# Optimization experiments

Measured on AMD Instinct MI355X. Metric: run time of the kernel, lower is better.

## Reference

```python
import jax, jax.numpy as jnp
import numpy as np

BATCH = 131072
INPUT_DIM = 256
HIDDEN = 128
DIM = 16
TRIL = DIM * (DIM + 1) // 2  # 136


def setup_inputs() -> dict:
    key = jax.random.key(0)
    k_x, k_w1, k_w2 = jax.random.split(key, 3)
    x = jax.random.normal(k_x, (BATCH, INPUT_DIM), dtype=jnp.float32)
    # Kaiming-ish init scaling so activations are well-conditioned
    W1 = jax.random.normal(k_w1, (INPUT_DIM, HIDDEN), dtype=jnp.float32) * (1.0 / np.sqrt(INPUT_DIM))
    b1 = jnp.zeros((HIDDEN,), dtype=jnp.float32)
    W2 = jax.random.normal(k_w2, (HIDDEN, TRIL), dtype=jnp.float32) * (1.0 / np.sqrt(HIDDEN))
    b2 = jnp.zeros((TRIL,), dtype=jnp.float32)
    return {"x": x, "W1": W1, "b1": b1, "W2": W2, "b2": b2}


def reference(x, W1, b1, W2, b2):
    # MLP: Linear -> ReLU -> Linear, producing tril entries of Cholesky factor
    h = jax.nn.relu(x @ W1 + b1)              # [B, 128]
    v = h @ W2 + b2                           # [B, 136]
    ti, tj = jnp.tril_indices(DIM)            # row-major tril order, matches torch.tril_indices
    L = jnp.zeros((x.shape[0], DIM, DIM), dtype=v.dtype).at[:, ti, tj].set(v)  # [B, D, D]
    rho = jnp.einsum('bik,bjk->bij', L, L)    # L @ L^T (real, so conj is no-op)
    trace = jnp.einsum('bii->b', rho)         # diagonal sum
    return rho / trace[:, None, None]
```

## Files before the change

kernel.cpp:

```cpp
#include <hip/hip_runtime.h>


typedef _Float16 h8 __attribute__((ext_vector_type(8)));
typedef float    f4 __attribute__((ext_vector_type(4)));
typedef int      i2 __attribute__((ext_vector_type(2)));

#define BATCH_N 131072
#define IN_DIM  256
#define HID     128
#define TRILN   136
#define BM      128
#define NT1     8
#define KS1     8
#define NT2     9
#define KS2     4
#define HSTR    136
#define LVSTR   160
#define PW1_N   (KS1*NT1*64*8)
#define PW2_N   (KS2*NT2*64*8)

__device__ __forceinline__ int rowoff(int i) {
    int g = i >> 2;
    return 4 * (g + 1) * (2 * g + (i & 3));
}

__global__ void pack_weights(const float* __restrict__ W1,
                             const float* __restrict__ W2,
                             _Float16* __restrict__ pw1,
                             _Float16* __restrict__ pw2) {
    int gid = blockIdx.x * blockDim.x + threadIdx.x;
    if (gid < PW1_N) {
        int j = gid & 7, l = (gid >> 3) & 63, f = gid >> 9;
        int ks = f >> 3, nt = f & 7;
        int k = ks * 32 + (l >> 4) * 8 + j;
        int n = nt * 16 + (l & 15);
        pw1[gid] = (_Float16)W1[k * HID + n];
    } else if (gid < PW1_N + PW2_N) {
        int g = gid - PW1_N;
        int j = g & 7, l = (g >> 3) & 63, f = g >> 9;
        int ks = f / NT2, nt = f - ks * NT2;
        int k = ks * 32 + (l >> 4) * 8 + j;
        int col = nt * 16 + (l & 15);
        pw2[g] = (col < TRILN) ? (_Float16)W2[k * TRILN + col] : (_Float16)0.0f;
    }
}

__device__ __forceinline__ h8 cvt_h8(f4 lo, f4 hi) {
    h8 r;
    r[0] = (_Float16)lo[0]; r[1] = (_Float16)lo[1];
    r[2] = (_Float16)lo[2]; r[3] = (_Float16)lo[3];
    r[4] = (_Float16)hi[0]; r[5] = (_Float16)hi[1];
    r[6] = (_Float16)hi[2]; r[7] = (_Float16)hi[3];
    return r;
}

__global__ __launch_bounds__(256, 4) void fused_mlp(
        const float* __restrict__ x, const float* __restrict__ b1,
        const float* __restrict__ b2, const _Float16* __restrict__ pw1,
        const _Float16* __restrict__ pw2, float* __restrict__ out) {
    __shared__ char smem_raw[BM * LVSTR * 2] __attribute__((aligned(16)));
    _Float16* hbuf = (_Float16*)smem_raw;
    _Float16* lv   = (_Float16*)smem_raw;

    const int tid  = threadIdx.x;
    const int w    = tid >> 6;
    const int lane = tid & 63;
    const int q    = lane >> 4;
    const int lm   = lane & 15;
    const int b0   = blockIdx.x * BM;

    f4 acc1[2][NT1];
    #pragma unroll
    for (int mt = 0; mt < 2; ++mt)
        #pragma unroll
        for (int nt = 0; nt < NT1; ++nt)
            acc1[mt][nt] = (f4){0.f, 0.f, 0.f, 0.f};

    const float* xr0 = x + (size_t)(b0 + w * 16 + lm) * IN_DIM + q * 8;
    const float* xr1 = xr0 + (size_t)64 * IN_DIM;

    f4 a0l = *(const f4*)xr0, a0h = *(const f4*)(xr0 + 4);
    f4 a1l = *(const f4*)xr1, a1h = *(const f4*)(xr1 + 4);

    #pragma unroll
    for (int ks = 0; ks < KS1; ++ks) {
        h8 bf[NT1];
        #pragma unroll
        for (int nt = 0; nt < NT1; ++nt)
            bf[nt] = *(const h8*)(pw1 + ((ks * NT1 + nt) * 64 + lane) * 8);
        h8 af0 = cvt_h8(a0l, a0h);
        h8 af1 = cvt_h8(a1l, a1h);
        if (ks + 1 < KS1) {
            const float* p0 = xr0 + (ks + 1) * 32;
            const float* p1 = xr1 + (ks + 1) * 32;
            a0l = *(const f4*)p0; a0h = *(const f4*)(p0 + 4);
            a1l = *(const f4*)p1; a1h = *(const f4*)(p1 + 4);
        }
        #pragma unroll
        for (int nt = 0; nt < NT1; ++nt) {
            acc1[0][nt] = __builtin_amdgcn_mfma_f32_16x16x32_f16(af0, bf[nt], acc1[0][nt], 0, 0, 0);
            acc1[1][nt] = __builtin_amdgcn_mfma_f32_16x16x32_f16(af1, bf[nt], acc1[1][nt], 0, 0, 0);
        }
    }

    {
        float b1v[NT1];
        #pragma unroll
        for (int nt = 0; nt < NT1; ++nt) b1v[nt] = b1[nt * 16 + lm];
        #pragma unroll
        for (int mt = 0; mt < 2; ++mt)
            #pragma unroll
            for (int nt = 0; nt < NT1; ++nt)
                #pragma unroll
                for (int r = 0; r < 4; ++r) {
                    float hv = acc1[mt][nt][r] + b1v[nt];
                    hv = fmaxf(hv, 0.f);
                    hbuf[(mt * 64 + w * 16 + q * 4 + r) * HSTR + nt * 16 + lm] = (_Float16)hv;
                }
    }

    f4 acc2[2][NT2];
    #pragma unroll
    for (int mt = 0; mt < 2; ++mt)
        #pragma unroll
        for (int nt = 0; nt < NT2; ++nt)
            acc2[mt][nt] = (f4){0.f, 0.f, 0.f, 0.f};

    #pragma unroll
    for (int ks = 0; ks < KS2; ++ks) {
        h8 ha0 = *(const h8*)(hbuf + (w * 16 + lm) * HSTR + ks * 32 + q * 8);
        h8 ha1 = *(const h8*)(hbuf + (64 + w * 16 + lm) * HSTR + ks * 32 + q * 8);
        #pragma unroll
        for (int nt = 0; nt < NT2; ++nt) {
            h8 bf = *(const h8*)(pw2 + ((ks * NT2 + nt) * 64 + lane) * 8);
            acc2[0][nt] = __builtin_amdgcn_mfma_f32_16x16x32_f16(ha0, bf, acc2[0][nt], 0, 0, 0);
            acc2[1][nt] = __builtin_amdgcn_mfma_f32_16x16x32_f16(ha1, bf, acc2[1][nt], 0, 0, 0);
        }
    }

    float b2v[NT2];
    #pragma unroll
    for (int nt = 0; nt < NT2; ++nt) {
        int col = nt * 16 + lm;
        b2v[nt] = (col < TRILN) ? b2[col] : 0.f;
    }

    float ps[2][4];
    #pragma unroll
    for (int mt = 0; mt < 2; ++mt)
        #pragma unroll
        for (int r = 0; r < 4; ++r) ps[mt][r] = 0.f;
    #pragma unroll
    for (int mt = 0; mt < 2; ++mt)
        #pragma unroll
        for (int nt = 0; nt < NT2; ++nt)
            #pragma unroll
            for (int r = 0; r < 4; ++r) {
                float v = acc2[mt][nt][r] + b2v[nt];
                ps[mt][r] += v * v;
            }

    float rinv[2][4];
    #pragma unroll
    for (int mt = 0; mt < 2; ++mt)
        #pragma unroll
        for (int r = 0; r < 4; ++r) {
            float s = ps[mt][r];
            s += __shfl_xor(s, 1);
            s += __shfl_xor(s, 2);
            s += __shfl_xor(s, 4);
            s += __shfl_xor(s, 8);
            rinv[mt][r] = 1.0f / s;
        }

    int voff[NT2];
    bool vok[NT2];
    #pragma unroll
    for (int nt = 0; nt < NT2; ++nt) {
        int c = nt * 16 + lm;
        vok[nt] = (c < TRILN);
        int cc = vok[nt] ? c : 0;
        int i = (int)((sqrtf(8.0f * (float)cc + 1.0f) - 1.0f) * 0.5f);
        int k = cc - (i * (i + 1)) / 2;
        voff[nt] = rowoff(i) + k;
    }

    __syncthreads();

    #pragma unroll
    for (int mt = 0; mt < 2; ++mt)
        #pragma unroll
        for (int r = 0; r < 4; ++r) {
            int base = (mt * 64 + w * 16 + q * 4 + r) * LVSTR;
            #pragma unroll
            for (int nt = 0; nt < NT2; ++nt)
                if (vok[nt])
                    lv[base + voff[nt]] = (_Float16)(acc2[mt][nt][r] + b2v[nt]);
        }

    int msk[4];
    {
        int n = lm - q * 8 + 1;
        #pragma unroll
        for (int p = 0; p < 4; ++p) {
            int c2 = n - 2 * p; c2 = c2 < 0 ? 0 : (c2 > 2 ? 2 : c2);
            msk[p] = (c2 == 2) ? ~0 : ((c2 == 1) ? 0xFFFF : 0);
        }
    }
    const int ro_lm = rowoff(lm);
    const f4 zero = (f4){0.f, 0.f, 0.f, 0.f};
    const int outcol = q * 64 + lm;

    #pragma unroll
    for (int mt = 0; mt < 2; ++mt)
        #pragma unroll
        for (int tq = 0; tq < 4; ++tq)
            #pragma unroll
            for (int r4 = 0; r4 < 4; ++r4) {
                int t = tq * 4 + r4;
                int row = mt * 64 + w * 16 + t;
                const _Float16* rp = lv + row * LVSTR + ro_lm + q * 8;
                i2 lo = *(const i2*)rp;
                i2 hi = *(const i2*)(rp + 4);
                h8 frag;
                ((i2*)&frag)[0] = (i2){lo.x & msk[0], lo.y & msk[1]};
                ((i2*)&frag)[1] = (i2){hi.x & msk[2], hi.y & msk[3]};
                f4 d = __builtin_amdgcn_mfma_f32_16x16x32_f16(frag, frag, zero, 0, 0, 0);
                float riv = __uint_as_float(
                    __builtin_amdgcn_readlane(__float_as_uint(rinv[mt][r4]), tq * 16));
                float* op = out + (size_t)(b0 + row) * 256 + outcol;
                #pragma unroll
                for (int sr = 0; sr < 4; ++sr)
                    op[sr * 16] = d[sr] * riv;
            }
}

extern "C" void kernel_launch(void* const* d_in, const int* in_sizes, int n_in,
                              void* d_out, int out_size, void* d_ws, size_t ws_size,
                              hipStream_t stream) {
    const float* x  = (const float*)d_in[0];
    const float* W1 = (const float*)d_in[1];
    const float* b1 = (const float*)d_in[2];
    const float* W2 = (const float*)d_in[3];
    const float* b2 = (const float*)d_in[4];
    float* out = (float*)d_out;

    _Float16* pw1 = (_Float16*)d_ws;
    _Float16* pw2 = pw1 + PW1_N;

    pack_weights<<<(PW1_N + PW2_N + 255) / 256, 256, 0, stream>>>(W1, W2, pw1, pw2);
    fused_mlp<<<BATCH_N / BM, 256, 0, stream>>>(x, b1, b2, pw1, pw2, out);
}
```

Baseline: 263.8 us.

## Halve block tile to 64 rows with per-wave private LDS and no barrier

Shrinks the batch tile from 128 to 64 rows so each wave handles one 16-row M-tile instead of two, halving accumulator registers and raising the launch-bounds occupancy hint from 4 to 5. Each wave gets its own private LDS chunk for the hidden activations and the scattered L matrix, which removes the block-wide __syncthreads. The hidden fragments are preloaded for all K steps. The trade-off is that each W1/W2 fragment load now feeds only one MFMA instead of two, doubling weight-fragment traffic per row.

```diff
diff --git a/kernel.cpp b/kernel.cpp
--- a/kernel.cpp
+++ b/kernel.cpp
@@ -9,13 +9,14 @@
 #define IN_DIM  256
 #define HID     128
 #define TRILN   136
-#define BM      128
+#define BM      64
 #define NT1     8
 #define KS1     8
 #define NT2     9
 #define KS2     4
 #define HSTR    136
 #define LVSTR   160
+#define CHUNKH  (16*LVSTR)
 #define PW1_N   (KS1*NT1*64*8)
 #define PW2_N   (KS2*NT2*64*8)
 
@@ -54,13 +55,11 @@
     return r;
 }
 
-__global__ __launch_bounds__(256, 4) void fused_mlp(
+__global__ __launch_bounds__(256, 5) void fused_mlp(
         const float* __restrict__ x, const float* __restrict__ b1,
         const float* __restrict__ b2, const _Float16* __restrict__ pw1,
         const _Float16* __restrict__ pw2, float* __restrict__ out) {
-    __shared__ char smem_raw[BM * LVSTR * 2] __attribute__((aligned(16)));
-    _Float16* hbuf = (_Float16*)smem_raw;
-    _Float16* lv   = (_Float16*)smem_raw;
+    __shared__ _Float16 smem[4 * CHUNKH] __attribute__((aligned(16)));
 
     const int tid  = threadIdx.x;
     const int w    = tid >> 6;
@@ -69,18 +68,15 @@
     const int lm   = lane & 15;
     const int b0   = blockIdx.x * BM;
 
-    f4 acc1[2][NT1];
-    #pragma unroll
-    for (int mt = 0; mt < 2; ++mt)
-        #pragma unroll
-        for (int nt = 0; nt < NT1; ++nt)
-            acc1[mt][nt] = (f4){0.f, 0.f, 0.f, 0.f};
+    _Float16* hbuf = smem + w * CHUNKH;
+    _Float16* lv   = smem + w * CHUNKH;
+
+    f4 acc1[NT1];
+    #pragma unroll
+    for (int nt = 0; nt < NT1; ++nt) acc1[nt] = (f4){0.f, 0.f, 0.f, 0.f};
 
     const float* xr0 = x + (size_t)(b0 + w * 16 + lm) * IN_DIM + q * 8;
-    const float* xr1 = xr0 + (size_t)64 * IN_DIM;
-
     f4 a0l = *(const f4*)xr0, a0h = *(const f4*)(xr0 + 4);
-    f4 a1l = *(const f4*)xr1, a1h = *(const f4*)(xr1 + 4);
 
     #pragma unroll
     for (int ks = 0; ks < KS1; ++ks) {
@@ -89,18 +85,13 @@
         for (int nt = 0; nt < NT1; ++nt)
             bf[nt] = *(const h8*)(pw1 + ((ks * NT1 + nt) * 64 + lane) * 8);
         h8 af0 = cvt_h8(a0l, a0h);
-        h8 af1 = cvt_h8(a1l, a1h);
         if (ks + 1 < KS1) {
             const float* p0 = xr0 + (ks + 1) * 32;
-            const float* p1 = xr1 + (ks + 1) * 32;
             a0l = *(const f4*)p0; a0h = *(const f4*)(p0 + 4);
-            a1l = *(const f4*)p1; a1h = *(const f4*)(p1 + 4);
-        }
-        #pragma unroll
-        for (int nt = 0; nt < NT1; ++nt) {
-            acc1[0][nt] = __builtin_amdgcn_mfma_f32_16x16x32_f16(af0, bf[nt], acc1[0][nt], 0, 0, 0);
-            acc1[1][nt] = __builtin_amdgcn_mfma_f32_16x16x32_f16(af1, bf[nt], acc1[1][nt], 0, 0, 0);
-        }
+        }
+        #pragma unroll
+        for (int nt = 0; nt < NT1; ++nt)
+            acc1[nt] = __builtin_amdgcn_mfma_f32_16x16x32_f16(af0, bf[nt], acc1[nt], 0, 0, 0);
     }
 
     {
@@ -108,33 +99,29 @@
         #pragma unroll
         for (int nt = 0; nt < NT1; ++nt) b1v[nt] = b1[nt * 16 + lm];
         #pragma unroll
-        for (int mt = 0; mt < 2; ++mt)
+        for (int nt = 0; nt < NT1; ++nt)
             #pragma unroll
-            for (int nt = 0; nt < NT1; ++nt)
-                #pragma unroll
-                for (int r = 0; r < 4; ++r) {
-                    float hv = acc1[mt][nt][r] + b1v[nt];
-                    hv = fmaxf(hv, 0.f);
-                    hbuf[(mt * 64 + w * 16 + q * 4 + r) * HSTR + nt * 16 + lm] = (_Float16)hv;
-                }
-    }
-
-    f4 acc2[2][NT2];
-    #pragma unroll
-    for (int mt = 0; mt < 2; ++mt)
-        #pragma unroll
-        for (int nt = 0; nt < NT2; ++nt)
-            acc2[mt][nt] = (f4){0.f, 0.f, 0.f, 0.f};
-
-    #pragma unroll
-    for (int ks = 0; ks < KS2; ++ks) {
-        h8 ha0 = *(const h8*)(hbuf + (w * 16 + lm) * HSTR + ks * 32 + q * 8);
-        h8 ha1 = *(const h8*)(hbuf + (64 + w * 16 + lm) * HSTR + ks * 32 + q * 8);
-        #pragma unroll
-        for (int nt = 0; nt < NT2; ++nt) {
+            for (int r = 0; r < 4; ++r) {
+                float hv = fmaxf(acc1[nt][r] + b1v[nt], 0.f);
+                hbuf[(q * 4 + r) * HSTR + nt * 16 + lm] = (_Float16)hv;
+            }
+    }
+
+    f4 acc2[NT2];
+    #pragma unroll
+    for (int nt = 0; nt < NT2; ++nt) acc2[nt] = (f4){0.f, 0.f, 0.f, 0.f};
+
+    h8 ha[KS2];
+    #pragma unroll
+    for (int ks = 0; ks < KS2; ++ks)
+        ha[ks] = *(const h8*)(hbuf + lm * HSTR + ks * 32 + q * 8);
+
+    #pragma unroll
+    for (int nt = 0; nt < NT2; ++nt) {
+        #pragma unroll
+        for (int ks = 0; ks < KS2; ++ks) {
             h8 bf = *(const h8*)(pw2 + ((ks * NT2 + nt) * 64 + lane) * 8);
-            acc2[0][nt] = __builtin_amdgcn_mfma_f32_16x16x32_f16(ha0, bf, acc2[0][nt], 0, 0, 0);
-            acc2[1][nt] = __builtin_amdgcn_mfma_f32_16x16x32_f16(ha1, bf, acc2[1][nt], 0, 0, 0);
+            acc2[nt] = __builtin_amdgcn_mfma_f32_16x16x32_f16(ha[ks], bf, acc2[nt], 0, 0, 0);
         }
     }
 
@@ -145,33 +132,26 @@
         b2v[nt] = (col < TRILN) ? b2[col] : 0.f;
     }
 
-    float ps[2][4];
-    #pragma unroll
-    for (int mt = 0; mt < 2; ++mt)
-        #pragma unroll
-        for (int r = 0; r < 4; ++r) ps[mt][r] = 0.f;
-    #pragma unroll
-    for (int mt = 0; mt < 2; ++mt)
+    float rinv[4];
+    {
+        float ps[4] = {0.f, 0.f, 0.f, 0.f};
         #pragma unroll
         for (int nt = 0; nt < NT2; ++nt)
             #pragma unroll
             for (int r = 0; r < 4; ++r) {
-                float v = acc2[mt][nt][r] + b2v[nt];
-                ps[mt][r] += v * v;
+                float v = acc2[nt][r] + b2v[nt];
+                ps[r] += v * v;
             }
-
-    float rinv[2][4];
-    #pragma unroll
-    for (int mt = 0; mt < 2; ++mt)
         #pragma unroll
         for (int r = 0; r < 4; ++r) {
-            float s = ps[mt][r];
+            float s = ps[r];
             s += __shfl_xor(s, 1);
             s += __shfl_xor(s, 2);
             s += __shfl_xor(s, 4);
             s += __shfl_xor(s, 8);
-            rinv[mt][r] = 1.0f / s;
-        }
+            rinv[r] = 1.0f / s;
+        }
+    }
 
     int voff[NT2];
     bool vok[NT2];
@@ -185,18 +165,14 @@
         voff[nt] = rowoff(i) + k;
     }
 
-    __syncthreads();
-
-    #pragma unroll
-    for (int mt = 0; mt < 2; ++mt)
-        #pragma unroll
-        for (int r = 0; r < 4; ++r) {
-            int base = (mt * 64 + w * 16 + q * 4 + r) * LVSTR;
-            #pragma unroll
-            for (int nt = 0; nt < NT2; ++nt)
-                if (vok[nt])
-                    lv[base + voff[nt]] = (_Float16)(acc2[mt][nt][r] + b2v[nt]);
-        }
+    #pragma unroll
+    for (int r = 0; r < 4; ++r) {
+        int base = (q * 4 + r) * LVSTR;
+        #pragma unroll
+        for (int nt = 0; nt < NT2; ++nt)
+            if (vok[nt])
+                lv[base + voff[nt]] = (_Float16)(acc2[nt][r] + b2v[nt]);
+    }
 
     int msk[4];
     {
@@ -212,27 +188,24 @@
     const int outcol = q * 64 + lm;
 
     #pragma unroll
-    for (int mt = 0; mt < 2; ++mt)
-        #pragma unroll
-        for (int tq = 0; tq < 4; ++tq)
+    for (int tq = 0; tq < 4; ++tq)
+        #pragma unroll
+        for (int r4 = 0; r4 < 4; ++r4) {
+            int t = tq * 4 + r4;
+            const _Float16* rp = lv + t * LVSTR + ro_lm + q * 8;
+            i2 lo = *(const i2*)rp;
+            i2 hi = *(const i2*)(rp + 4);
+            h8 frag;
+            ((i2*)&frag)[0] = (i2){lo.x & msk[0], lo.y & msk[1]};
+            ((i2*)&frag)[1] = (i2){hi.x & msk[2], hi.y & msk[3]};
+            f4 d = __builtin_amdgcn_mfma_f32_16x16x32_f16(frag, frag, zero, 0, 0, 0);
+            float riv = __uint_as_float(
+                __builtin_amdgcn_readlane(__float_as_uint(rinv[r4]), tq * 16));
+            float* op = out + (size_t)(b0 + w * 16 + t) * 256 + outcol;
             #pragma unroll
-            for (int r4 = 0; r4 < 4; ++r4) {
-                int t = tq * 4 + r4;
-                int row = mt * 64 + w * 16 + t;
-                const _Float16* rp = lv + row * LVSTR + ro_lm + q * 8;
-                i2 lo = *(const i2*)rp;
-                i2 hi = *(const i2*)(rp + 4);
-                h8 frag;
-                ((i2*)&frag)[0] = (i2){lo.x & msk[0], lo.y & msk[1]};
-                ((i2*)&frag)[1] = (i2){hi.x & msk[2], hi.y & msk[3]};
-                f4 d = __builtin_amdgcn_mfma_f32_16x16x32_f16(frag, frag, zero, 0, 0, 0);
-                float riv = __uint_as_float(
-                    __builtin_amdgcn_readlane(__float_as_uint(rinv[mt][r4]), tq * 16));
-                float* op = out + (size_t)(b0 + row) * 256 + outcol;
-                #pragma unroll
-                for (int sr = 0; sr < 4; ++sr)
-                    op[sr * 16] = d[sr] * riv;
-            }
+            for (int sr = 0; sr < 4; ++sr)
+                op[sr * 16] = d[sr] * riv;
+        }
 }
 
 extern "C" void kernel_launch(void* const* d_in, const int* in_sizes, int n_in,
```

New measurement: 269.3 us. 1.02x slower.
